# Performance work log

Hardware: AMD Instinct MI355X
Metric: run time of the kernel (lower is better)

Reference implementation:

```python
import jax, jax.numpy as jnp
import numpy as np

B, S, D, H, DH = 4, 2048, 1024, 16, 64
SCALE = 1.0 / (DH ** 0.5)
LN_EPS = 1e-5


def setup_inputs() -> dict:
    key = jax.random.key(0)
    ks = jax.random.split(key, 5)
    h = jax.random.normal(ks[0], (B, S, D), dtype=jnp.float32)
    # torch init: normal(0, scale). We store weights as (in, out) and apply x @ W,
    # which is distributionally identical to torch's x @ W.T with random weights.
    Wq = SCALE * jax.random.normal(ks[1], (D, H * DH), dtype=jnp.float32)
    Wk = SCALE * jax.random.normal(ks[2], (D, H * DH), dtype=jnp.float32)
    Wv = SCALE * jax.random.normal(ks[3], (D, H * DH), dtype=jnp.float32)
    Wo = SCALE * jax.random.normal(ks[4], (H * DH, D), dtype=jnp.float32)
    gamma = jnp.ones((D,), dtype=jnp.float32)
    beta = jnp.zeros((D,), dtype=jnp.float32)
    return {"h": h, "Wq": Wq, "Wk": Wk, "Wv": Wv, "Wo": Wo,
            "gamma": gamma, "beta": beta}


def _layer_norm(x, gamma, beta):
    mu = jnp.mean(x, axis=-1, keepdims=True)
    var = jnp.mean(jnp.square(x - mu), axis=-1, keepdims=True)
    return gamma * (x - mu) * jax.lax.rsqrt(var + LN_EPS) + beta


def reference(h, Wq, Wk, Wv, Wo, gamma, beta):
    b, s, d = h.shape
    # Q/K/V projections (no bias), reshaped to [b, s, n_head, d_head]
    q = (h @ Wq).reshape(b, s, H, DH)
    k = (h @ Wk).reshape(b, s, H, DH)  # mems=None -> c == h
    v = (h @ Wv).reshape(b, s, H, DH)
    # attn_score: [b, i, j, n], scaled
    scores = jnp.einsum('bind,bjnd->bijn', q, k) * SCALE
    # softmax over key axis j (dim=2), no mask (attn_mask=None)
    probs = jax.nn.softmax(scores, axis=2)
    attn_vec = jnp.einsum('bijn,bjnd->bind', probs, v).reshape(b, s, H * DH)
    attn_out = attn_vec @ Wo  # dropout=0 (eval)
    # post-LayerNorm residual (pre_lnorm=False)
    return _layer_norm(h + attn_out, gamma, beta)
```

## Files before the change

kernel.cpp:

```cpp
#include <hip/hip_runtime.h>
#include <hip/hip_bf16.h>


typedef __attribute__((ext_vector_type(8))) _Float16 half8;
typedef __attribute__((ext_vector_type(4))) _Float16 half4;
typedef __attribute__((ext_vector_type(4))) float f32x4;

#define D_MODEL 1024
#define SEQ     2048
#define NHEAD   16
#define HDIM    64
#define NTOK    8192

__device__ __forceinline__ void gload_lds16(const _Float16* g, _Float16* l) {
  __builtin_amdgcn_global_load_lds(
      (const __attribute__((address_space(1))) void*)g,
      (__attribute__((address_space(3))) void*)l, 16, 0, 0);
}

template<int ROWS>
__device__ __forceinline__ void stage_swz(const _Float16* __restrict__ g, int ldg,
                                          _Float16* lds, int t) {
  int lane = t & 63, w = t >> 6;
  int rr = lane >> 3, gcol = lane & 7;
#pragma unroll
  for (int i = 0; i < ROWS / 32; ++i) {
    int rowbase = i * 32 + w * 8;
    int row = rowbase + rr;
    int gsw = gcol ^ (row & 7);
    gload_lds16(g + (size_t)row * ldg + gsw * 8, lds + rowbase * 64);
  }
}

__device__ __forceinline__ half8 lds_frag(const _Float16* base, int row, int kk, int lane) {
  int gg = (kk * 4 + (lane >> 4)) ^ (row & 7);
  return *(const half8*)(base + row * 64 + gg * 8);
}

__global__ __launch_bounds__(256)
void wtrans(const float* __restrict__ Wq, const float* __restrict__ Wk,
            const float* __restrict__ Wv, const float* __restrict__ Wo,
            _Float16* __restrict__ outAll) {
  __shared__ float tile[64][65];
  int z = blockIdx.z;
  const float* W = (z == 0) ? Wq : (z == 1) ? Wk : (z == 2) ? Wv : Wo;
  float scale = (z == 0) ? 0.125f : 1.0f;
  _Float16* out = outAll + (size_t)z * D_MODEL * D_MODEL;
  int n0 = blockIdx.x * 64, k0 = blockIdx.y * 64;
  int t = threadIdx.x, c = t & 63, rq = t >> 6;
#pragma unroll
  for (int i = 0; i < 16; ++i) {
    int r = rq * 16 + i;
    tile[r][c] = W[(size_t)(k0 + r) * D_MODEL + n0 + c];
  }
  __syncthreads();
#pragma unroll
  for (int i = 0; i < 16; ++i) {
    int r = rq * 16 + i;
    out[(size_t)(n0 + r) * D_MODEL + k0 + c] = (_Float16)(tile[c][r] * scale);
  }
}

__global__ __launch_bounds__(256)
void cvt_h(const float* __restrict__ in, _Float16* __restrict__ out) {
  int i = (blockIdx.x * 256 + threadIdx.x) * 4;
  float4 v = *(const float4*)&in[i];
  half4 o;
  o[0] = (_Float16)v.x; o[1] = (_Float16)v.y;
  o[2] = (_Float16)v.z; o[3] = (_Float16)v.w;
  *(half4*)&out[i] = o;
}

__global__ __launch_bounds__(256, 2)
void gemm_tn(const _Float16* __restrict__ A, const _Float16* __restrict__ BtBase,
             _Float16* __restrict__ CBase, size_t strideB, size_t strideC) {
  constexpr int N = D_MODEL, K = D_MODEL;
  const _Float16* Bt = BtBase + strideB * blockIdx.z;
  _Float16* C = CBase + strideC * blockIdx.z;
  __shared__ __align__(16) _Float16 As[2][128 * 64];
  __shared__ __align__(16) _Float16 Bs[2][128 * 64];
  int t = threadIdx.x, lane = t & 63, w = t >> 6;
  int wr = w >> 1, wc = w & 1;
  const _Float16* Ab = A + (size_t)blockIdx.y * 128 * K;
  const _Float16* Bb = Bt + (size_t)blockIdx.x * 128 * K;

  f32x4 acc[4][4];
#pragma unroll
  for (int m = 0; m < 4; ++m)
#pragma unroll
    for (int n = 0; n < 4; ++n) acc[m][n] = f32x4{0.f, 0.f, 0.f, 0.f};

  stage_swz<128>(Ab, K, As[0], t);
  stage_swz<128>(Bb, K, Bs[0], t);
  __syncthreads();

  constexpr int NT = K / 64;
  for (int kt = 0; kt < NT; ++kt) {
    int cur = kt & 1;
    if (kt + 1 < NT) {
      stage_swz<128>(Ab + (kt + 1) * 64, K, As[cur ^ 1], t);
      stage_swz<128>(Bb + (kt + 1) * 64, K, Bs[cur ^ 1], t);
    }
#pragma unroll
    for (int kk = 0; kk < 2; ++kk) {
      half8 af[4], bf[4];
#pragma unroll
      for (int m = 0; m < 4; ++m)
        af[m] = lds_frag(As[cur], wr * 64 + m * 16 + (lane & 15), kk, lane);
#pragma unroll
      for (int n = 0; n < 4; ++n)
        bf[n] = lds_frag(Bs[cur], wc * 64 + n * 16 + (lane & 15), kk, lane);
#pragma unroll
      for (int m = 0; m < 4; ++m)
#pragma unroll
        for (int n = 0; n < 4; ++n)
          acc[m][n] = __builtin_amdgcn_mfma_f32_16x16x32_f16(af[m], bf[n], acc[m][n], 0, 0, 0);
    }
    __syncthreads();
  }

#pragma unroll
  for (int m = 0; m < 4; ++m)
#pragma unroll
    for (int n = 0; n < 4; ++n)
#pragma unroll
      for (int r = 0; r < 4; ++r) {
        int row = blockIdx.y * 128 + wr * 64 + m * 16 + (lane >> 4) * 4 + r;
        int col = blockIdx.x * 128 + wc * 64 + n * 16 + (lane & 15);
        C[(size_t)row * N + col] = (_Float16)acc[m][n][r];
      }
}

__global__ __launch_bounds__(256, 2)
void attn(const _Float16* __restrict__ Q, const _Float16* __restrict__ Kg,
          const _Float16* __restrict__ V, _Float16* __restrict__ Ovec) {
  __shared__ __align__(16) _Float16 Ks[64 * 64];
  __shared__ __align__(16) _Float16 Vt[64 * 64];
  int t = threadIdx.x, lane = t & 63, w = t >> 6;
  int g = lane >> 4, c = lane & 15;
  int q0 = blockIdx.x * 64;
  int bh = blockIdx.y, b = bh >> 4, h = bh & 15;
  size_t base = ((size_t)b * SEQ) * D_MODEL + h * HDIM;

  half8 aQ[2];
  {
    int row = q0 + w * 16 + c;
    const _Float16* qp = Q + base + (size_t)row * D_MODEL;
#pragma unroll
    for (int kk = 0; kk < 2; ++kk) aQ[kk] = *(const half8*)&qp[kk * 32 + 8 * g];
  }

  float mr = -1e30f, lr = 0.f;
  f32x4 accO[4];
#pragma unroll
  for (int n = 0; n < 4; ++n) accO[n] = f32x4{0.f, 0.f, 0.f, 0.f};

  for (int kv0 = 0; kv0 < SEQ; kv0 += 64) {
    __syncthreads();
    stage_swz<64>(Kg + base + (size_t)kv0 * D_MODEL, D_MODEL, Ks, t);
    {
      const _Float16* vp = V + base + (size_t)(kv0 + lane) * D_MODEL + 8 * w;
      half8 vv0 = *(const half8*)vp;
      half8 vv1 = *(const half8*)(vp + 32);
      int tw = (lane >> 2) ^ ((w & 1) * 8);
      int l3 = lane & 3;
      int d0 = 8 * w;
#pragma unroll
      for (int j = 0; j < 8; ++j) {
        int col = ((tw ^ j) << 2) + l3;
        Vt[(d0 + j) * 64 + col] = vv0[j];
        Vt[(d0 + 32 + j) * 64 + col] = vv1[j];
      }
    }
    __syncthreads();

    f32x4 s[4];
#pragma unroll
    for (int n = 0; n < 4; ++n) s[n] = f32x4{0.f, 0.f, 0.f, 0.f};
#pragma unroll
    for (int kk = 0; kk < 2; ++kk)
#pragma unroll
      for (int n = 0; n < 4; ++n) {
        half8 aK = lds_frag(Ks, n * 16 + c, kk, lane);
        s[n] = __builtin_amdgcn_mfma_f32_16x16x32_f16(aK, aQ[kk], s[n], 0, 0, 0);
      }

    float vmax = s[0][0];
#pragma unroll
    for (int n = 0; n < 4; ++n)
#pragma unroll
      for (int r = 0; r < 4; ++r) vmax = fmaxf(vmax, s[n][r]);
    vmax = fmaxf(vmax, __shfl_xor(vmax, 16, 64));
    vmax = fmaxf(vmax, __shfl_xor(vmax, 32, 64));
    float mnew = fmaxf(mr, vmax);
    float sc = __expf(mr - mnew);
    float p[4][4];
    float lsum = 0.f;
#pragma unroll
    for (int n = 0; n < 4; ++n)
#pragma unroll
      for (int r = 0; r < 4; ++r) {
        float e = __expf(s[n][r] - mnew);
        p[n][r] = e; lsum += e;
      }
    lsum += __shfl_xor(lsum, 16, 64);
    lsum += __shfl_xor(lsum, 32, 64);
    lr = lr * sc + lsum;
    mr = mnew;
    float scq[4];
#pragma unroll
    for (int r = 0; r < 4; ++r) scq[r] = __shfl(sc, 4 * g + r, 64);
#pragma unroll
    for (int n = 0; n < 4; ++n)
#pragma unroll
      for (int r = 0; r < 4; ++r) accO[n][r] *= scq[r];

    half8 aP[2];
#pragma unroll
    for (int kk = 0; kk < 2; ++kk)
#pragma unroll
      for (int j = 0; j < 8; ++j)
        aP[kk][j] = (_Float16)p[2 * kk + (j >> 2)][j & 3];

#pragma unroll
    for (int kk = 0; kk < 2; ++kk)
#pragma unroll
      for (int n = 0; n < 4; ++n) {
        const _Float16* rowp = Vt + (size_t)(16 * n + c) * 64;
        half4 lo = *(const half4*)&rowp[((8 * kk + g) ^ c) << 2];
        half4 hi = *(const half4*)&rowp[((8 * kk + 4 + g) ^ c) << 2];
        half8 bV;
#pragma unroll
        for (int j = 0; j < 4; ++j) { bV[j] = lo[j]; bV[4 + j] = hi[j]; }
        accO[n] = __builtin_amdgcn_mfma_f32_16x16x32_f16(aP[kk], bV, accO[n], 0, 0, 0);
      }
  }

  float lrq[4];
#pragma unroll
  for (int r = 0; r < 4; ++r) lrq[r] = __shfl(lr, 4 * g + r, 64);
#pragma unroll
  for (int n = 0; n < 4; ++n)
#pragma unroll
    for (int r = 0; r < 4; ++r) {
      int row = q0 + w * 16 + 4 * g + r;
      Ovec[base + (size_t)row * D_MODEL + n * 16 + c] =
          (_Float16)(accO[n][r] / lrq[r]);
    }
}

__global__ __launch_bounds__(256)
void ln_res(const float* __restrict__ h, const _Float16* __restrict__ ao,
            const float* __restrict__ gamma, const float* __restrict__ beta,
            float* __restrict__ out) {
  int row = blockIdx.x;
  int t = threadIdx.x, lane = t & 63, w = t >> 6;
  const float* hp = h + (size_t)row * D_MODEL;
  const _Float16* ap = ao + (size_t)row * D_MODEL;
  float4 hv = *(const float4*)&hp[t * 4];
  half4 av = *(const half4*)&ap[t * 4];
  float x[4];
  x[0] = hv.x + (float)av[0]; x[1] = hv.y + (float)av[1];
  x[2] = hv.z + (float)av[2]; x[3] = hv.w + (float)av[3];
  float sum = x[0] + x[1] + x[2] + x[3];
  float ssq = x[0]*x[0] + x[1]*x[1] + x[2]*x[2] + x[3]*x[3];
#pragma unroll
  for (int off = 1; off < 64; off <<= 1) {
    sum += __shfl_xor(sum, off, 64);
    ssq += __shfl_xor(ssq, off, 64);
  }
  __shared__ float rs[4], rq[4];
  if (lane == 0) { rs[w] = sum; rq[w] = ssq; }
  __syncthreads();
  sum = rs[0] + rs[1] + rs[2] + rs[3];
  ssq = rq[0] + rq[1] + rq[2] + rq[3];
  float mu = sum * (1.f / 1024.f);
  float var = ssq * (1.f / 1024.f) - mu * mu;
  float inv = rsqrtf(var + 1e-5f);
  float4 gv = *(const float4*)&gamma[t * 4];
  float4 bv = *(const float4*)&beta[t * 4];
  float4 ov;
  ov.x = (x[0] - mu) * inv * gv.x + bv.x;
  ov.y = (x[1] - mu) * inv * gv.y + bv.y;
  ov.z = (x[2] - mu) * inv * gv.z + bv.z;
  ov.w = (x[3] - mu) * inv * gv.w + bv.w;
  *(float4*)&out[(size_t)row * D_MODEL + t * 4] = ov;
}

extern "C" void kernel_launch(void* const* d_in, const int* in_sizes, int n_in,
                              void* d_out, int out_size, void* d_ws, size_t ws_size,
                              hipStream_t stream) {
  const float* h     = (const float*)d_in[0];
  const float* Wq    = (const float*)d_in[1];
  const float* Wk    = (const float*)d_in[2];
  const float* Wv    = (const float*)d_in[3];
  const float* Wo    = (const float*)d_in[4];
  const float* gamma = (const float*)d_in[5];
  const float* beta  = (const float*)d_in[6];
  float* out = (float*)d_out;

  char* ws = (char*)d_ws;
  _Float16* WT  = (_Float16*)ws;
  _Float16* X   = (_Float16*)(ws + (size_t)8  * 1024 * 1024);
  _Float16* QKV = (_Float16*)(ws + (size_t)24 * 1024 * 1024);
  const size_t WSTRIDE = (size_t)D_MODEL * D_MODEL;
  const size_t CSTRIDE = (size_t)NTOK * D_MODEL;

  wtrans<<<dim3(16, 16, 4), 256, 0, stream>>>(Wq, Wk, Wv, Wo, WT);
  cvt_h<<<dim3(NTOK * D_MODEL / 1024), 256, 0, stream>>>(h, X);
  gemm_tn<<<dim3(8, 64, 3), 256, 0, stream>>>(X, WT, QKV, WSTRIDE, CSTRIDE);
  attn<<<dim3(SEQ / 64, 64), 256, 0, stream>>>(QKV, QKV + CSTRIDE, QKV + 2 * CSTRIDE, X);
  gemm_tn<<<dim3(8, 64, 1), 256, 0, stream>>>(X, WT + 3 * WSTRIDE, QKV, 0, 0);
  ln_res<<<dim3(NTOK), 256, 0, stream>>>(h, QKV, gamma, beta, out);

  (void)in_sizes; (void)n_in; (void)out_size; (void)ws_size;
}
```

Before: 352.6 us.

## Double-buffer K/V tiles in attention and use exp2 with lazy rescaling

The attention loop now uses two LDS buffers for K and V. The next tile's K is prefetched via global_load_lds and its V is loaded into registers while the current tile is being computed, which leaves one barrier per iteration instead of two. Softmax now uses raw v_exp_f32 (exp2), with log2(e) folded into the Q weight scale. The running max and the accumulator are only rescaled when the max grows by more than 8, which skips most rescale work. LDS use doubles, which may affect the occupancy target of 2 blocks, and the lazy rescale lets probabilities exceed 1, up to about 2^8, before fp16 conversion.

```diff
diff --git a/kernel.cpp b/kernel.cpp
--- a/kernel.cpp
+++ b/kernel.cpp
@@ -35,6 +35,12 @@
 __device__ __forceinline__ half8 lds_frag(const _Float16* base, int row, int kk, int lane) {
   int gg = (kk * 4 + (lane >> 4)) ^ (row & 7);
   return *(const half8*)(base + row * 64 + gg * 8);
+}
+
+__device__ __forceinline__ float fast_exp2(float x) {
+  float r;
+  asm("v_exp_f32 %0, %1" : "=v"(r) : "v"(x));
+  return r;
 }
 
 __global__ __launch_bounds__(256)
@@ -44,7 +50,7 @@
   __shared__ float tile[64][65];
   int z = blockIdx.z;
   const float* W = (z == 0) ? Wq : (z == 1) ? Wk : (z == 2) ? Wv : Wo;
-  float scale = (z == 0) ? 0.125f : 1.0f;
+  float scale = (z == 0) ? 0.125f * 1.4426950408889634f : 1.0f;
   _Float16* out = outAll + (size_t)z * D_MODEL * D_MODEL;
   int n0 = blockIdx.x * 64, k0 = blockIdx.y * 64;
   int t = threadIdx.x, c = t & 63, rq = t >> 6;
@@ -134,8 +140,8 @@
 __global__ __launch_bounds__(256, 2)
 void attn(const _Float16* __restrict__ Q, const _Float16* __restrict__ Kg,
           const _Float16* __restrict__ V, _Float16* __restrict__ Ovec) {
-  __shared__ __align__(16) _Float16 Ks[64 * 64];
-  __shared__ __align__(16) _Float16 Vt[64 * 64];
+  __shared__ __align__(16) _Float16 Ks[2][64 * 64];
+  __shared__ __align__(16) _Float16 Vt[2][64 * 64];
   int t = threadIdx.x, lane = t & 63, w = t >> 6;
   int g = lane >> 4, c = lane & 15;
   int q0 = blockIdx.x * 64;
@@ -150,29 +156,40 @@
     for (int kk = 0; kk < 2; ++kk) aQ[kk] = *(const half8*)&qp[kk * 32 + 8 * g];
   }
 
+  const int tw = (lane >> 2) ^ ((w & 1) * 8);
+  const int l3 = lane & 3;
+  const int d0v = 8 * w;
+
   float mr = -1e30f, lr = 0.f;
   f32x4 accO[4];
 #pragma unroll
   for (int n = 0; n < 4; ++n) accO[n] = f32x4{0.f, 0.f, 0.f, 0.f};
 
-  for (int kv0 = 0; kv0 < SEQ; kv0 += 64) {
-    __syncthreads();
-    stage_swz<64>(Kg + base + (size_t)kv0 * D_MODEL, D_MODEL, Ks, t);
-    {
-      const _Float16* vp = V + base + (size_t)(kv0 + lane) * D_MODEL + 8 * w;
-      half8 vv0 = *(const half8*)vp;
-      half8 vv1 = *(const half8*)(vp + 32);
-      int tw = (lane >> 2) ^ ((w & 1) * 8);
-      int l3 = lane & 3;
-      int d0 = 8 * w;
-#pragma unroll
-      for (int j = 0; j < 8; ++j) {
-        int col = ((tw ^ j) << 2) + l3;
-        Vt[(d0 + j) * 64 + col] = vv0[j];
-        Vt[(d0 + 32 + j) * 64 + col] = vv1[j];
-      }
-    }
-    __syncthreads();
+  stage_swz<64>(Kg + base, D_MODEL, Ks[0], t);
+  {
+    const _Float16* vp = V + base + (size_t)lane * D_MODEL + d0v;
+    half8 vv0 = *(const half8*)vp;
+    half8 vv1 = *(const half8*)(vp + 32);
+#pragma unroll
+    for (int j = 0; j < 8; ++j) {
+      int col = ((tw ^ j) << 2) + l3;
+      Vt[0][(d0v + j) * 64 + col] = vv0[j];
+      Vt[0][(d0v + 32 + j) * 64 + col] = vv1[j];
+    }
+  }
+  __syncthreads();
+
+  for (int tix = 0; tix < SEQ / 64; ++tix) {
+    int cur = tix & 1;
+    int kv0 = tix * 64;
+    bool pf = (tix + 1 < SEQ / 64);
+    half8 vv0, vv1;
+    if (pf) {
+      stage_swz<64>(Kg + base + (size_t)(kv0 + 64) * D_MODEL, D_MODEL, Ks[cur ^ 1], t);
+      const _Float16* vp = V + base + (size_t)(kv0 + 64 + lane) * D_MODEL + d0v;
+      vv0 = *(const half8*)vp;
+      vv1 = *(const half8*)(vp + 32);
+    }
 
     f32x4 s[4];
 #pragma unroll
@@ -181,7 +198,7 @@
     for (int kk = 0; kk < 2; ++kk)
 #pragma unroll
       for (int n = 0; n < 4; ++n) {
-        half8 aK = lds_frag(Ks, n * 16 + c, kk, lane);
+        half8 aK = lds_frag(Ks[cur], n * 16 + c, kk, lane);
         s[n] = __builtin_amdgcn_mfma_f32_16x16x32_f16(aK, aQ[kk], s[n], 0, 0, 0);
       }
 
@@ -192,28 +209,40 @@
       for (int r = 0; r < 4; ++r) vmax = fmaxf(vmax, s[n][r]);
     vmax = fmaxf(vmax, __shfl_xor(vmax, 16, 64));
     vmax = fmaxf(vmax, __shfl_xor(vmax, 32, 64));
-    float mnew = fmaxf(mr, vmax);
-    float sc = __expf(mr - mnew);
+    if (__any(vmax - mr > 8.f)) {
+      float mnew = fmaxf(mr, vmax);
+      float sc = fast_exp2(mr - mnew);
+      lr *= sc;
+      float scq[4];
+#pragma unroll
+      for (int r = 0; r < 4; ++r) scq[r] = __shfl(sc, 4 * g + r, 64);
+#pragma unroll
+      for (int n = 0; n < 4; ++n)
+#pragma unroll
+        for (int r = 0; r < 4; ++r) accO[n][r] *= scq[r];
+      mr = mnew;
+    }
     float p[4][4];
     float lsum = 0.f;
 #pragma unroll
     for (int n = 0; n < 4; ++n)
 #pragma unroll
       for (int r = 0; r < 4; ++r) {
-        float e = __expf(s[n][r] - mnew);
+        float e = fast_exp2(s[n][r] - mr);
         p[n][r] = e; lsum += e;
       }
     lsum += __shfl_xor(lsum, 16, 64);
     lsum += __shfl_xor(lsum, 32, 64);
-    lr = lr * sc + lsum;
-    mr = mnew;
-    float scq[4];
-#pragma unroll
-    for (int r = 0; r < 4; ++r) scq[r] = __shfl(sc, 4 * g + r, 64);
-#pragma unroll
-    for (int n = 0; n < 4; ++n)
-#pragma unroll
-      for (int r = 0; r < 4; ++r) accO[n][r] *= scq[r];
+    lr += lsum;
+
+    if (pf) {
+#pragma unroll
+      for (int j = 0; j < 8; ++j) {
+        int col = ((tw ^ j) << 2) + l3;
+        Vt[cur ^ 1][(d0v + j) * 64 + col] = vv0[j];
+        Vt[cur ^ 1][(d0v + 32 + j) * 64 + col] = vv1[j];
+      }
+    }
 
     half8 aP[2];
 #pragma unroll
@@ -226,7 +255,7 @@
     for (int kk = 0; kk < 2; ++kk)
 #pragma unroll
       for (int n = 0; n < 4; ++n) {
-        const _Float16* rowp = Vt + (size_t)(16 * n + c) * 64;
+        const _Float16* rowp = Vt[cur] + (size_t)(16 * n + c) * 64;
         half4 lo = *(const half4*)&rowp[((8 * kk + g) ^ c) << 2];
         half4 hi = *(const half4*)&rowp[((8 * kk + 4 + g) ^ c) << 2];
         half8 bV;
@@ -234,6 +263,7 @@
         for (int j = 0; j < 4; ++j) { bV[j] = lo[j]; bV[4 + j] = hi[j]; }
         accO[n] = __builtin_amdgcn_mfma_f32_16x16x32_f16(aP[kk], bV, accO[n], 0, 0, 0);
       }
+    __syncthreads();
   }
 
   float lrq[4];
```

Measured after the change: 354.6 us. About the same (+0.6%).
